# Performance work log

Hardware: AMD Instinct MI355X
Metric: run time of the kernel (lower is better)

## Reference

```python
import jax, jax.numpy as jnp
import numpy as np

B, V, D = 512, 50000, 512   # batch, vocab, embedding_dim
T, P, L, PL = 4, 16, 8, 32  # max_types, max_paths, max_pathlen, max_prop_len
OUT = 300


def masked_softmax(x):
    # zeros are treated as padding: add -9999 before softmax
    return jax.nn.softmax(x + jnp.where(x == 0, -9999.0, 0.0), axis=-1)


def cosine(a, b, eps=1e-8):
    na = jnp.maximum(jnp.linalg.norm(a, axis=1), eps)
    nb = jnp.maximum(jnp.linalg.norm(b, axis=1), eps)
    return jnp.sum(a * b, axis=1) / (na * nb)


def setup_inputs() -> dict:
    key = jax.random.key(0)
    ks = jax.random.split(key, 10)
    nodes = jax.random.randint(ks[0], (B, 2), 0, V)
    features = jax.random.randint(ks[1], (B, 2, T, P, L), 0, V)
    prop_nodes = jax.random.randint(ks[2], (B, 2), 0, V)
    prop_features = jax.random.randint(ks[3], (B, 2, 3, PL), 0, V)
    emb = jax.random.normal(ks[4], (V, D), dtype=jnp.float32)
    W_out = jax.random.normal(ks[5], (OUT, 2 * D), dtype=jnp.float32) * (1.0 / np.sqrt(2 * D))
    b_out = jnp.zeros((OUT,), dtype=jnp.float32)
    v = jnp.full((L,), 1.0 / L, dtype=jnp.float32)
    w_rootpath = jnp.array([0.25], dtype=jnp.float32)
    w_children = jnp.array([0.25], dtype=jnp.float32)
    w_obj_neighbours = jnp.array([0.25], dtype=jnp.float32)
    prop_weight = jnp.array([0.33], dtype=jnp.float32)
    domain_weight = jnp.array([0.33], dtype=jnp.float32)
    return dict(nodes=nodes, features=features, prop_nodes=prop_nodes,
                prop_features=prop_features, emb=emb, W_out=W_out, b_out=b_out,
                v=v, w_rootpath=w_rootpath, w_children=w_children,
                w_obj_neighbours=w_obj_neighbours, prop_weight=prop_weight,
                domain_weight=domain_weight)


def reference(nodes, features, prop_nodes, prop_features, emb, W_out, b_out,
              v, w_rootpath, w_children, w_obj_neighbours, prop_weight,
              domain_weight):
    results = []
    for i in range(2):  # the two siamese branches
        node_emb = emb[nodes[:, i]]                      # [B, D]
        feature_emb = emb[features[:, i]]                # [B, T, P, L, D]
        # score each path: dot every token with the node embedding, sum over pathlen
        path_weights = jnp.einsum('bd,btpld->btp', node_emb, feature_emb)  # [B,T,P]
        best = jnp.argmax(path_weights, axis=-1)         # [B, T]
        best_path = jnp.take_along_axis(
            feature_emb, best[:, :, None, None, None], axis=2).squeeze(2)  # [B,T,L,D]
        node_weights = masked_softmax(
            jnp.einsum('bd,btld->btl', node_emb, best_path))               # [B,T,L]
        attended = node_weights[..., None] * best_path                     # [B,T,L,D]
        dwp = jnp.einsum('l,btld->btd', v, attended)                       # [B,T,D]
        w_data = 1.0 - w_rootpath - w_children - w_obj_neighbours
        context = (w_rootpath * dwp[:, 0] + w_children * dwp[:, 1]
                   + w_obj_neighbours * dwp[:, 2] + w_data * dwp[:, 3])    # [B,D]
        contextual = jnp.concatenate([node_emb, context], axis=1)          # [B,2D]
        results.append(contextual @ W_out.T + b_out)                       # [B,300]
    sim_ent = cosine(results[0], results[1])                               # [B]
    # property branch (prop_nodes non-empty here)
    agg = emb[prop_features].sum(axis=-2)                                  # [B,2,3,D]
    sim_prop = (prop_weight * cosine(agg[:, 0, 0], agg[:, 1, 0])
                + domain_weight * cosine(agg[:, 0, 1], agg[:, 1, 1])
                + (1.0 - prop_weight - domain_weight) * cosine(agg[:, 0, 2], agg[:, 1, 2]))
    return jnp.concatenate([sim_ent, sim_prop])                            # [2B]
```

## Files before the change

kernel.cpp:

```cpp
#include <hip/hip_runtime.h>
#include <math.h>

#define B_ 512
#define V_ 50000
#define D_ 512
#define T_ 4
#define P_ 16
#define L_ 8
#define OUT_ 300
#define NBI 1024
#define NG  4096
#define NSLOT 524288
#define NSCAN 196

__global__ __launch_bounds__(256) void kprep(
    const int* __restrict__ features, int* __restrict__ counts,
    const int* __restrict__ nodes, const float* __restrict__ emb,
    float* __restrict__ narr, const float* __restrict__ W,
    float4* __restrict__ Wtv)
{
    const int blk = blockIdx.x;
    const int tid = threadIdx.x;
    if (blk < NSLOT / 256) {
        const int slot = blk * 256 + tid;
        atomicAdd(&counts[features[slot]], 1);
    } else if (blk < NSLOT / 256 + NBI) {
        const int bi = blk - NSLOT / 256;
        const float2 r = *(const float2*)(emb + (size_t)nodes[bi] * D_ + 2 * tid);
        *(float2*)(narr + (size_t)bi * D_ + 2 * tid) = r;
    } else {
        const int o = blk - NSLOT / 256 - NBI;
        const float4 w = *(const float4*)(W + (size_t)o * 1024 + 4 * tid);
        Wtv[(size_t)tid * OUT_ + o] = w;
    }
}

__global__ __launch_bounds__(256) void kb1_bsum(
    const int* __restrict__ counts, int* __restrict__ bsum)
{
    const int tid = threadIdx.x, v = blockIdx.x * 256 + tid;
    const int wid = tid >> 6, lane = tid & 63;
    __shared__ int red[4];
    int c = (v < V_) ? counts[v] : 0;
    #pragma unroll
    for (int off = 32; off; off >>= 1) c += __shfl_down(c, off);
    if (lane == 0) red[wid] = c;
    __syncthreads();
    if (tid == 0) bsum[blockIdx.x] = red[0] + red[1] + red[2] + red[3];
}

__global__ __launch_bounds__(256) void kb2_scan(
    const int* __restrict__ bsum, int* __restrict__ bbase)
{
    const int tid = threadIdx.x;
    __shared__ int sc[256];
    const int x = (tid < NSCAN) ? bsum[tid] : 0;
    sc[tid] = x;
    __syncthreads();
    for (int off = 1; off < 256; off <<= 1) {
        const int y = (tid >= off) ? sc[tid - off] : 0;
        __syncthreads();
        sc[tid] += y;
        __syncthreads();
    }
    if (tid < NSCAN) bbase[tid] = sc[tid] - x;
}

__global__ __launch_bounds__(256) void kb3_offsets(
    const int* __restrict__ counts, const int* __restrict__ bbase,
    int* __restrict__ offs, int* __restrict__ cursor)
{
    const int tid = threadIdx.x, v = blockIdx.x * 256 + tid;
    __shared__ int sc[256];
    const int c = (v < V_) ? counts[v] : 0;
    sc[tid] = c;
    __syncthreads();
    for (int off = 1; off < 256; off <<= 1) {
        const int y = (tid >= off) ? sc[tid - off] : 0;
        __syncthreads();
        sc[tid] += y;
        __syncthreads();
    }
    const int o = bbase[blockIdx.x] + sc[tid] - c;
    if (v < V_) { offs[v] = o; cursor[v] = o; }
    if (v == V_ - 1) offs[V_] = o + c;
}

__global__ __launch_bounds__(256) void kc_scatter(
    const int* __restrict__ features, int* __restrict__ cursor,
    int* __restrict__ inv)
{
    const int slot = blockIdx.x * 256 + threadIdx.x;
    const int row  = features[slot];
    const int pos  = atomicAdd(&cursor[row], 1);
    inv[pos] = slot;
}

__global__ __launch_bounds__(256) void kd_dots(
    const float* __restrict__ emb, const float* __restrict__ narr,
    const int* __restrict__ offs, const int* __restrict__ inv,
    float* __restrict__ sarr)
{
    const int tid = threadIdx.x;
    const int wid = tid >> 6, lane = tid & 63;
    const int row = blockIdx.x * 4 + wid;
    const int st = offs[row], en = offs[row + 1];
    if (st >= en) return;

    const float* rp = emb + (size_t)row * D_ + lane * 8;
    const float4 r0 = ((const float4*)rp)[0];
    const float4 r1 = ((const float4*)rp)[1];

    const int grp = lane >> 4;
    const int sub = lane & 15;
    const int eperm = (grp == 1) ? 2 : (grp == 2) ? 1 : grp;

    for (int e = st; e < en; e += 4) {
        int  s[4]; bool val[4];
        #pragma unroll
        for (int k = 0; k < 4; ++k) {
            val[k] = (e + k) < en;
            s[k]   = inv[val[k] ? (e + k) : (en - 1)];
        }
        float d[4];
        #pragma unroll
        for (int k = 0; k < 4; ++k) {
            const float* q = narr + (size_t)(s[k] >> 9) * D_ + lane * 8;
            const float4 a0 = ((const float4*)q)[0];
            const float4 a1 = ((const float4*)q)[1];
            d[k] = r0.x*a0.x + r0.y*a0.y + r0.z*a0.z + r0.w*a0.w
                 + r1.x*a1.x + r1.y*a1.y + r1.z*a1.z + r1.w*a1.w;
        }
        const bool b32 = (lane & 32) != 0;
        float c01 = (b32 ? d[1] : d[0]) + __shfl_xor(b32 ? d[0] : d[1], 32);
        float c23 = (b32 ? d[3] : d[2]) + __shfl_xor(b32 ? d[2] : d[3], 32);
        const bool b16 = (lane & 16) != 0;
        float c = (b16 ? c23 : c01) + __shfl_xor(b16 ? c01 : c23, 16);
        c += __shfl_xor(c, 8);
        c += __shfl_xor(c, 4);
        c += __shfl_xor(c, 2);
        c += __shfl_xor(c, 1);
        if (sub == 0 && val[eperm]) sarr[s[eperm]] = c;
    }
}

__global__ __launch_bounds__(256) void kef_sel_ctx(
    const float* __restrict__ sarr, const int* __restrict__ features,
    const int* __restrict__ nodes, const float* __restrict__ emb,
    const float* __restrict__ v, const float* __restrict__ w_rp,
    const float* __restrict__ w_ch, const float* __restrict__ w_on,
    float* __restrict__ cont)
{
    const int bi  = blockIdx.x;
    const int tid = threadIdx.x;
    const int wid = tid >> 6, lane = tid & 63;
    const int g = bi * 4 + wid;
    const int t = wid;

    __shared__ int   s_idx[32];
    __shared__ float s_coef[32];

    float bv = -1e30f; int bix = 0x7fffffff;
    if (lane < P_) {
        const float* sp = sarr + (size_t)g * 128 + lane * 8;
        const float4 x0 = ((const float4*)sp)[0];
        const float4 x1 = ((const float4*)sp)[1];
        bv = x0.x + x0.y + x0.z + x0.w + x1.x + x1.y + x1.z + x1.w;
        bix = lane;
    }
    #pragma unroll
    for (int off = 8; off; off >>= 1) {
        const float ov = __shfl_down(bv, off);
        const int   oi = __shfl_down(bix, off);
        if (ov > bv || (ov == bv && oi < bix)) { bv = ov; bix = oi; }
    }
    const int bp = __shfl(bix, 0);

    float sv = 0.f;
    if (lane < L_) sv = sarr[(size_t)g * 128 + bp * 8 + lane];
    float x = sv + (sv == 0.0f ? -9999.0f : 0.0f);
    float m = x;
    #pragma unroll
    for (int off = 4; off; off >>= 1) m = fmaxf(m, __shfl_xor(m, off));
    const float e = expf(x - m);
    float sum = e;
    #pragma unroll
    for (int off = 4; off; off >>= 1) sum += __shfl_xor(sum, off);

    if (lane < L_) {
        const float wr = w_rp[0], wc = w_ch[0], wo = w_on[0];
        const float tw = (t == 0) ? wr : (t == 1) ? wc : (t == 2) ? wo
                                       : (1.0f - wr - wc - wo);
        s_coef[wid * 8 + lane] = tw * v[lane] * (e / sum);
        s_idx [wid * 8 + lane] = features[(size_t)g * 128 + bp * 8 + lane];
    }
    __syncthreads();

    float2 c = {0.f, 0.f};
    #pragma unroll 8
    for (int r = 0; r < 32; ++r) {
        const int   idx = s_idx[r];
        const float cf  = s_coef[r];
        const float2 rr = *(const float2*)(emb + (size_t)idx * D_ + 2 * tid);
        c.x += cf * rr.x;
        c.y += cf * rr.y;
    }
    const float2 nn = *(const float2*)(emb + (size_t)nodes[bi] * D_ + 2 * tid);
    float* cp = cont + (size_t)bi * 1024;
    *(float2*)(cp + 2 * tid)       = nn;
    *(float2*)(cp + 512 + 2 * tid) = c;
}

__global__ __launch_bounds__(256) void kg_gemm_cos(
    const float* __restrict__ cont, const float4* __restrict__ Wtv,
    const float* __restrict__ bias, float* __restrict__ out)
{
    const int bb  = blockIdx.x;
    const int tid = threadIdx.x;
    const int wid = tid >> 6, lane = tid & 63;

    __shared__ float4 cs[1024];
    __shared__ float  red[4][6];

    const float* cb = cont + (size_t)bb * 4 * 1024;
    for (int idx = tid; idx < 4096; idx += 256) {
        const int vv = idx & 3, k = idx >> 2;
        ((float*)&cs[k])[vv] = cb[vv * 1024 + k];
    }
    __syncthreads();

    float p[6] = {0,0,0,0,0,0};
    #pragma unroll
    for (int pass = 0; pass < 2; ++pass) {
        const int o = tid + pass * 256;
        if (o < OUT_) {
            float4 acc = {0,0,0,0};
            const float4* wp = Wtv + o;
            #pragma unroll 4
            for (int k4 = 0; k4 < 256; ++k4) {
                const float4 wv = wp[(size_t)k4 * OUT_];
                const float4 c0 = cs[4*k4+0];
                const float4 c1 = cs[4*k4+1];
                const float4 c2 = cs[4*k4+2];
                const float4 c3 = cs[4*k4+3];
                acc.x += c0.x*wv.x + c1.x*wv.y + c2.x*wv.z + c3.x*wv.w;
                acc.y += c0.y*wv.x + c1.y*wv.y + c2.y*wv.z + c3.y*wv.w;
                acc.z += c0.z*wv.x + c1.z*wv.y + c2.z*wv.z + c3.z*wv.w;
                acc.w += c0.w*wv.x + c1.w*wv.y + c2.w*wv.z + c3.w*wv.w;
            }
            const float bo = bias[o];
            const float r0 = acc.x + bo, r1 = acc.y + bo;
            const float r2 = acc.z + bo, r3 = acc.w + bo;
            p[0] += r0 * r1; p[1] += r0 * r0; p[2] += r1 * r1;
            p[3] += r2 * r3; p[4] += r2 * r2; p[5] += r3 * r3;
        }
    }
    #pragma unroll
    for (int q = 0; q < 6; ++q) {
        #pragma unroll
        for (int off = 32; off; off >>= 1) p[q] += __shfl_down(p[q], off);
    }
    if (lane == 0) {
        #pragma unroll
        for (int q = 0; q < 6; ++q) red[wid][q] = p[q];
    }
    __syncthreads();
    if (tid < 2) {
        const int j = tid;
        float ab = 0.f, aa = 0.f, bbv = 0.f;
        #pragma unroll
        for (int w2 = 0; w2 < 4; ++w2) {
            ab  += red[w2][j*3+0];
            aa  += red[w2][j*3+1];
            bbv += red[w2][j*3+2];
        }
        const float na = fmaxf(sqrtf(aa),  1e-8f);
        const float nb = fmaxf(sqrtf(bbv), 1e-8f);
        out[bb * 2 + j] = ab / (na * nb);
    }
}

__global__ __launch_bounds__(256) void kh1_prop(
    const int* __restrict__ pf, const float* __restrict__ emb,
    float* __restrict__ pprt)
{
    const int bj  = blockIdx.x;
    const int b   = bj / 3, j = bj % 3;
    const int tid = threadIdx.x;
    const int d4   = tid & 127;
    const int half = tid >> 7;

    const int base0 = ((b * 2 + 0) * 3 + j) * 32;
    const int base1 = ((b * 2 + 1) * 3 + j) * 32;

    float4 accA = {0,0,0,0}, accB = {0,0,0,0};
    #pragma unroll 4
    for (int k = half; k < 32; k += 2) {
        const int ia = pf[base0 + k];
        const int ib = pf[base1 + k];
        const float4 ra = *(const float4*)(emb + (size_t)ia * D_ + 4 * d4);
        const float4 rb = *(const float4*)(emb + (size_t)ib * D_ + 4 * d4);
        accA.x += ra.x; accA.y += ra.y; accA.z += ra.z; accA.w += ra.w;
        accB.x += rb.x; accB.y += rb.y; accB.z += rb.z; accB.w += rb.w;
    }

    __shared__ float4 lA[128], lB[128];
    __shared__ float  red[2][3];
    if (half == 1) { lA[d4] = accA; lB[d4] = accB; }
    __syncthreads();

    float pab = 0.f, paa = 0.f, pbb = 0.f;
    if (half == 0) {
        const float4 oA = lA[d4], oB = lB[d4];
        const float ax = accA.x + oA.x, ay = accA.y + oA.y;
        const float az = accA.z + oA.z, aw = accA.w + oA.w;
        const float bx = accB.x + oB.x, by = accB.y + oB.y;
        const float bz = accB.z + oB.z, bw = accB.w + oB.w;
        pab = ax*bx + ay*by + az*bz + aw*bw;
        paa = ax*ax + ay*ay + az*az + aw*aw;
        pbb = bx*bx + by*by + bz*bz + bw*bw;
    }
    #pragma unroll
    for (int off = 32; off; off >>= 1) {
        pab += __shfl_down(pab, off);
        paa += __shfl_down(paa, off);
        pbb += __shfl_down(pbb, off);
    }
    if ((tid & 63) == 0 && tid < 128) {
        red[tid >> 6][0] = pab; red[tid >> 6][1] = paa; red[tid >> 6][2] = pbb;
    }
    __syncthreads();
    if (tid == 0) {
        pprt[bj * 3 + 0] = red[0][0] + red[1][0];
        pprt[bj * 3 + 1] = red[0][1] + red[1][1];
        pprt[bj * 3 + 2] = red[0][2] + red[1][2];
    }
}

__global__ __launch_bounds__(256) void kh2_prop(
    const float* __restrict__ pprt, const float* __restrict__ pw_,
    const float* __restrict__ dw_, float* __restrict__ out)
{
    const int b = blockIdx.x * 256 + threadIdx.x;
    if (b >= B_) return;
    float cosv[3];
    #pragma unroll
    for (int j = 0; j < 3; ++j) {
        const float ab = pprt[(b * 3 + j) * 3 + 0];
        const float aa = pprt[(b * 3 + j) * 3 + 1];
        const float bb = pprt[(b * 3 + j) * 3 + 2];
        const float na = fmaxf(sqrtf(aa), 1e-8f);
        const float nb = fmaxf(sqrtf(bb), 1e-8f);
        cosv[j] = ab / (na * nb);
    }
    const float pw = pw_[0], dw = dw_[0];
    out[B_ + b] = pw * cosv[0] + dw * cosv[1] + (1.0f - pw - dw) * cosv[2];
}

extern "C" void kernel_launch(void* const* d_in, const int* in_sizes, int n_in,
                              void* d_out, int out_size, void* d_ws, size_t ws_size,
                              hipStream_t stream) {
    const int*   nodes   = (const int*)  d_in[0];
    const int*   features= (const int*)  d_in[1];
    const int*   propf   = (const int*)  d_in[3];
    const float* emb     = (const float*)d_in[4];
    const float* W_out   = (const float*)d_in[5];
    const float* b_out   = (const float*)d_in[6];
    const float* v       = (const float*)d_in[7];
    const float* w_rp    = (const float*)d_in[8];
    const float* w_ch    = (const float*)d_in[9];
    const float* w_on    = (const float*)d_in[10];
    const float* pw      = (const float*)d_in[11];
    const float* dw      = (const float*)d_in[12];
    float* out = (float*)d_out;

    char* ws = (char*)d_ws;
    size_t o = 0;
    auto alloc = [&](size_t bytes) { char* p = ws + o; o += (bytes + 1023) & ~(size_t)1023; return p; };
    int*   counts = (int*)  alloc(V_ * 4);
    int*   offs   = (int*)  alloc((V_ + 1) * 4);
    int*   cursor = (int*)  alloc(V_ * 4);
    int*   bsum   = (int*)  alloc(NSCAN * 4);
    int*   bbase  = (int*)  alloc(NSCAN * 4);
    float* narr   = (float*)alloc((size_t)NBI * D_ * 4);
    int*   inv    = (int*)  alloc((size_t)NSLOT * 4);
    float* sarr   = (float*)alloc((size_t)NSLOT * 4);
    float* cont   = (float*)alloc((size_t)NBI * 1024 * 4);
    float* pprt   = (float*)alloc(B_ * 3 * 3 * 4);
    float4* Wtv   = (float4*)alloc((size_t)256 * OUT_ * 16);

    hipMemsetAsync(counts, 0, V_ * 4, stream);
    kprep      <<<NSLOT/256 + NBI + OUT_, 256, 0, stream>>>(
                  features, counts, nodes, emb, narr, W_out, Wtv);
    kb1_bsum   <<<NSCAN,      256, 0, stream>>>(counts, bsum);
    kb2_scan   <<<1,          256, 0, stream>>>(bsum, bbase);
    kb3_offsets<<<NSCAN,      256, 0, stream>>>(counts, bbase, offs, cursor);
    kc_scatter <<<NSLOT/256,  256, 0, stream>>>(features, cursor, inv);
    kd_dots    <<<V_/4,       256, 0, stream>>>(emb, narr, offs, inv, sarr);
    kef_sel_ctx<<<NBI,        256, 0, stream>>>(sarr, features, nodes, emb,
                                                v, w_rp, w_ch, w_on, cont);
    kg_gemm_cos<<<B_/2,       256, 0, stream>>>(cont, Wtv, b_out, out);
    kh1_prop   <<<B_*3,       256, 0, stream>>>(propf, emb, pprt);
    kh2_prop   <<<2,          256, 0, stream>>>(pprt, pw, dw, out);
}
```

Baseline: 235.2 us.

## Fuse property-branch kernels into dots and GEMM launches, unroll dot loop by eight

The property-sum kernel is merged into the per-row dot kernel as extra leading blocks, and the final property cosine kernel is merged into the GEMM/cosine kernel as two extra blocks. This removes two launches and lets the property gathers overlap with the dot-product work. The dot loop now handles eight entries per iteration, issuing all loads before computing, to raise memory-level parallelism. The cost is higher register pressure and shared memory that the dots path reserves but never uses.

```diff
diff --git a/kernel.cpp b/kernel.cpp
--- a/kernel.cpp
+++ b/kernel.cpp
@@ -12,6 +12,7 @@
 #define NG  4096
 #define NSLOT 524288
 #define NSCAN 196
+#define NPROPB 1536
 
 __global__ __launch_bounds__(256) void kprep(
     const int* __restrict__ features, int* __restrict__ counts,
@@ -96,14 +97,71 @@
     inv[pos] = slot;
 }
 
-__global__ __launch_bounds__(256) void kd_dots(
+__global__ __launch_bounds__(256) void kdh_dots_prop(
     const float* __restrict__ emb, const float* __restrict__ narr,
     const int* __restrict__ offs, const int* __restrict__ inv,
-    float* __restrict__ sarr)
-{
+    float* __restrict__ sarr,
+    const int* __restrict__ pf, float* __restrict__ pprt)
+{
+    const int blk = blockIdx.x;
     const int tid = threadIdx.x;
+
+    __shared__ float4 lA[128], lB[128];
+    __shared__ float  redp[2][3];
+
+    if (blk < NPROPB) {
+        const int bj  = blk;
+        const int b   = bj / 3, j = bj % 3;
+        const int d4   = tid & 127;
+        const int half = tid >> 7;
+
+        const int base0 = ((b * 2 + 0) * 3 + j) * 32;
+        const int base1 = ((b * 2 + 1) * 3 + j) * 32;
+
+        float4 accA = {0,0,0,0}, accB = {0,0,0,0};
+        #pragma unroll 4
+        for (int k = half; k < 32; k += 2) {
+            const int ia = pf[base0 + k];
+            const int ib = pf[base1 + k];
+            const float4 ra = *(const float4*)(emb + (size_t)ia * D_ + 4 * d4);
+            const float4 rb = *(const float4*)(emb + (size_t)ib * D_ + 4 * d4);
+            accA.x += ra.x; accA.y += ra.y; accA.z += ra.z; accA.w += ra.w;
+            accB.x += rb.x; accB.y += rb.y; accB.z += rb.z; accB.w += rb.w;
+        }
+        if (half == 1) { lA[d4] = accA; lB[d4] = accB; }
+        __syncthreads();
+
+        float pab = 0.f, paa = 0.f, pbb = 0.f;
+        if (half == 0) {
+            const float4 oA = lA[d4], oB = lB[d4];
+            const float ax = accA.x + oA.x, ay = accA.y + oA.y;
+            const float az = accA.z + oA.z, aw = accA.w + oA.w;
+            const float bx = accB.x + oB.x, by = accB.y + oB.y;
+            const float bz = accB.z + oB.z, bw = accB.w + oB.w;
+            pab = ax*bx + ay*by + az*bz + aw*bw;
+            paa = ax*ax + ay*ay + az*az + aw*aw;
+            pbb = bx*bx + by*by + bz*bz + bw*bw;
+        }
+        #pragma unroll
+        for (int off = 32; off; off >>= 1) {
+            pab += __shfl_down(pab, off);
+            paa += __shfl_down(paa, off);
+            pbb += __shfl_down(pbb, off);
+        }
+        if ((tid & 63) == 0 && tid < 128) {
+            redp[tid >> 6][0] = pab; redp[tid >> 6][1] = paa; redp[tid >> 6][2] = pbb;
+        }
+        __syncthreads();
+        if (tid == 0) {
+            pprt[bj * 3 + 0] = redp[0][0] + redp[1][0];
+            pprt[bj * 3 + 1] = redp[0][1] + redp[1][1];
+            pprt[bj * 3 + 2] = redp[0][2] + redp[1][2];
+        }
+        return;
+    }
+
     const int wid = tid >> 6, lane = tid & 63;
-    const int row = blockIdx.x * 4 + wid;
+    const int row = (blk - NPROPB) * 4 + wid;
     const int st = offs[row], en = offs[row + 1];
     if (st >= en) return;
 
@@ -115,32 +173,68 @@
     const int sub = lane & 15;
     const int eperm = (grp == 1) ? 2 : (grp == 2) ? 1 : grp;
 
-    for (int e = st; e < en; e += 4) {
-        int  s[4]; bool val[4];
+    for (int e = st; e < en; e += 8) {
+        const bool half2 = (e + 4) < en;
+        int  s0[4], s1[4]; bool v0[4], v1[4];
         #pragma unroll
         for (int k = 0; k < 4; ++k) {
-            val[k] = (e + k) < en;
-            s[k]   = inv[val[k] ? (e + k) : (en - 1)];
-        }
+            v0[k] = (e + k) < en;
+            s0[k] = inv[v0[k] ? (e + k) : (en - 1)];
+        }
+        #pragma unroll
+        for (int k = 0; k < 4; ++k) {
+            v1[k] = (e + 4 + k) < en;
+            s1[k] = inv[v1[k] ? (e + 4 + k) : (en - 1)];
+        }
+
+        float4 A0[4], A1[4], B0[4], B1[4];
+        #pragma unroll
+        for (int k = 0; k < 4; ++k) {
+            const float4* q = (const float4*)(narr + (size_t)(s0[k] >> 9) * D_ + lane * 8);
+            A0[k] = q[0]; A1[k] = q[1];
+        }
+        if (half2) {
+            #pragma unroll
+            for (int k = 0; k < 4; ++k) {
+                const float4* q = (const float4*)(narr + (size_t)(s1[k] >> 9) * D_ + lane * 8);
+                B0[k] = q[0]; B1[k] = q[1];
+            }
+        }
+
         float d[4];
         #pragma unroll
-        for (int k = 0; k < 4; ++k) {
-            const float* q = narr + (size_t)(s[k] >> 9) * D_ + lane * 8;
-            const float4 a0 = ((const float4*)q)[0];
-            const float4 a1 = ((const float4*)q)[1];
-            d[k] = r0.x*a0.x + r0.y*a0.y + r0.z*a0.z + r0.w*a0.w
-                 + r1.x*a1.x + r1.y*a1.y + r1.z*a1.z + r1.w*a1.w;
-        }
-        const bool b32 = (lane & 32) != 0;
-        float c01 = (b32 ? d[1] : d[0]) + __shfl_xor(b32 ? d[0] : d[1], 32);
-        float c23 = (b32 ? d[3] : d[2]) + __shfl_xor(b32 ? d[2] : d[3], 32);
-        const bool b16 = (lane & 16) != 0;
-        float c = (b16 ? c23 : c01) + __shfl_xor(b16 ? c01 : c23, 16);
-        c += __shfl_xor(c, 8);
-        c += __shfl_xor(c, 4);
-        c += __shfl_xor(c, 2);
-        c += __shfl_xor(c, 1);
-        if (sub == 0 && val[eperm]) sarr[s[eperm]] = c;
+        for (int k = 0; k < 4; ++k)
+            d[k] = r0.x*A0[k].x + r0.y*A0[k].y + r0.z*A0[k].z + r0.w*A0[k].w
+                 + r1.x*A1[k].x + r1.y*A1[k].y + r1.z*A1[k].z + r1.w*A1[k].w;
+        {
+            const bool b32 = (lane & 32) != 0;
+            float c01 = (b32 ? d[1] : d[0]) + __shfl_xor(b32 ? d[0] : d[1], 32);
+            float c23 = (b32 ? d[3] : d[2]) + __shfl_xor(b32 ? d[2] : d[3], 32);
+            const bool b16 = (lane & 16) != 0;
+            float c = (b16 ? c23 : c01) + __shfl_xor(b16 ? c01 : c23, 16);
+            c += __shfl_xor(c, 8);
+            c += __shfl_xor(c, 4);
+            c += __shfl_xor(c, 2);
+            c += __shfl_xor(c, 1);
+            if (sub == 0 && v0[eperm]) sarr[s0[eperm]] = c;
+        }
+        if (half2) {
+            float g[4];
+            #pragma unroll
+            for (int k = 0; k < 4; ++k)
+                g[k] = r0.x*B0[k].x + r0.y*B0[k].y + r0.z*B0[k].z + r0.w*B0[k].w
+                     + r1.x*B1[k].x + r1.y*B1[k].y + r1.z*B1[k].z + r1.w*B1[k].w;
+            const bool b32 = (lane & 32) != 0;
+            float c01 = (b32 ? g[1] : g[0]) + __shfl_xor(b32 ? g[0] : g[1], 32);
+            float c23 = (b32 ? g[3] : g[2]) + __shfl_xor(b32 ? g[2] : g[3], 32);
+            const bool b16 = (lane & 16) != 0;
+            float c = (b16 ? c23 : c01) + __shfl_xor(b16 ? c01 : c23, 16);
+            c += __shfl_xor(c, 8);
+            c += __shfl_xor(c, 4);
+            c += __shfl_xor(c, 2);
+            c += __shfl_xor(c, 1);
+            if (sub == 0 && v1[eperm]) sarr[s1[eperm]] = c;
+        }
     }
 }
 
@@ -213,10 +307,32 @@
 
 __global__ __launch_bounds__(256) void kg_gemm_cos(
     const float* __restrict__ cont, const float4* __restrict__ Wtv,
-    const float* __restrict__ bias, float* __restrict__ out)
+    const float* __restrict__ bias, const float* __restrict__ pprt,
+    const float* __restrict__ pw_, const float* __restrict__ dw_,
+    float* __restrict__ out)
 {
     const int bb  = blockIdx.x;
     const int tid = threadIdx.x;
+
+    if (bb >= B_ / 2) {
+        const int b = (bb - B_ / 2) * 256 + tid;
+        if (b < B_) {
+            float cosv[3];
+            #pragma unroll
+            for (int j = 0; j < 3; ++j) {
+                const float ab = pprt[(b * 3 + j) * 3 + 0];
+                const float aa = pprt[(b * 3 + j) * 3 + 1];
+                const float bv = pprt[(b * 3 + j) * 3 + 2];
+                const float na = fmaxf(sqrtf(aa), 1e-8f);
+                const float nb = fmaxf(sqrtf(bv), 1e-8f);
+                cosv[j] = ab / (na * nb);
+            }
+            const float pw = pw_[0], dw = dw_[0];
+            out[B_ + b] = pw * cosv[0] + dw * cosv[1] + (1.0f - pw - dw) * cosv[2];
+        }
+        return;
+    }
+
     const int wid = tid >> 6, lane = tid & 63;
 
     __shared__ float4 cs[1024];
@@ -280,83 +396,6 @@
     }
 }
 
-__global__ __launch_bounds__(256) void kh1_prop(
-    const int* __restrict__ pf, const float* __restrict__ emb,
-    float* __restrict__ pprt)
-{
-    const int bj  = blockIdx.x;
-    const int b   = bj / 3, j = bj % 3;
-    const int tid = threadIdx.x;
-    const int d4   = tid & 127;
-    const int half = tid >> 7;
-
-    const int base0 = ((b * 2 + 0) * 3 + j) * 32;
-    const int base1 = ((b * 2 + 1) * 3 + j) * 32;
-
-    float4 accA = {0,0,0,0}, accB = {0,0,0,0};
-    #pragma unroll 4
-    for (int k = half; k < 32; k += 2) {
-        const int ia = pf[base0 + k];
-        const int ib = pf[base1 + k];
-        const float4 ra = *(const float4*)(emb + (size_t)ia * D_ + 4 * d4);
-        const float4 rb = *(const float4*)(emb + (size_t)ib * D_ + 4 * d4);
-        accA.x += ra.x; accA.y += ra.y; accA.z += ra.z; accA.w += ra.w;
-        accB.x += rb.x; accB.y += rb.y; accB.z += rb.z; accB.w += rb.w;
-    }
-
-    __shared__ float4 lA[128], lB[128];
-    __shared__ float  red[2][3];
-    if (half == 1) { lA[d4] = accA; lB[d4] = accB; }
-    __syncthreads();
-
-    float pab = 0.f, paa = 0.f, pbb = 0.f;
-    if (half == 0) {
-        const float4 oA = lA[d4], oB = lB[d4];
-        const float ax = accA.x + oA.x, ay = accA.y + oA.y;
-        const float az = accA.z + oA.z, aw = accA.w + oA.w;
-        const float bx = accB.x + oB.x, by = accB.y + oB.y;
-        const float bz = accB.z + oB.z, bw = accB.w + oB.w;
-        pab = ax*bx + ay*by + az*bz + aw*bw;
-        paa = ax*ax + ay*ay + az*az + aw*aw;
-        pbb = bx*bx + by*by + bz*bz + bw*bw;
-    }
-    #pragma unroll
-    for (int off = 32; off; off >>= 1) {
-        pab += __shfl_down(pab, off);
-        paa += __shfl_down(paa, off);
-        pbb += __shfl_down(pbb, off);
-    }
-    if ((tid & 63) == 0 && tid < 128) {
-        red[tid >> 6][0] = pab; red[tid >> 6][1] = paa; red[tid >> 6][2] = pbb;
-    }
-    __syncthreads();
-    if (tid == 0) {
-        pprt[bj * 3 + 0] = red[0][0] + red[1][0];
-        pprt[bj * 3 + 1] = red[0][1] + red[1][1];
-        pprt[bj * 3 + 2] = red[0][2] + red[1][2];
-    }
-}
-
-__global__ __launch_bounds__(256) void kh2_prop(
-    const float* __restrict__ pprt, const float* __restrict__ pw_,
-    const float* __restrict__ dw_, float* __restrict__ out)
-{
-    const int b = blockIdx.x * 256 + threadIdx.x;
-    if (b >= B_) return;
-    float cosv[3];
-    #pragma unroll
-    for (int j = 0; j < 3; ++j) {
-        const float ab = pprt[(b * 3 + j) * 3 + 0];
-        const float aa = pprt[(b * 3 + j) * 3 + 1];
-        const float bb = pprt[(b * 3 + j) * 3 + 2];
-        const float na = fmaxf(sqrtf(aa), 1e-8f);
-        const float nb = fmaxf(sqrtf(bb), 1e-8f);
-        cosv[j] = ab / (na * nb);
-    }
-    const float pw = pw_[0], dw = dw_[0];
-    out[B_ + b] = pw * cosv[0] + dw * cosv[1] + (1.0f - pw - dw) * cosv[2];
-}
-
 extern "C" void kernel_launch(void* const* d_in, const int* in_sizes, int n_in,
                               void* d_out, int out_size, void* d_ws, size_t ws_size,
                               hipStream_t stream) {
@@ -390,16 +429,16 @@
     float4* Wtv   = (float4*)alloc((size_t)256 * OUT_ * 16);
 
     hipMemsetAsync(counts, 0, V_ * 4, stream);
-    kprep      <<<NSLOT/256 + NBI + OUT_, 256, 0, stream>>>(
-                  features, counts, nodes, emb, narr, W_out, Wtv);
-    kb1_bsum   <<<NSCAN,      256, 0, stream>>>(counts, bsum);
-    kb2_scan   <<<1,          256, 0, stream>>>(bsum, bbase);
-    kb3_offsets<<<NSCAN,      256, 0, stream>>>(counts, bbase, offs, cursor);
-    kc_scatter <<<NSLOT/256,  256, 0, stream>>>(features, cursor, inv);
-    kd_dots    <<<V_/4,       256, 0, stream>>>(emb, narr, offs, inv, sarr);
-    kef_sel_ctx<<<NBI,        256, 0, stream>>>(sarr, features, nodes, emb,
-                                                v, w_rp, w_ch, w_on, cont);
-    kg_gemm_cos<<<B_/2,       256, 0, stream>>>(cont, Wtv, b_out, out);
-    kh1_prop   <<<B_*3,       256, 0, stream>>>(propf, emb, pprt);
-    kh2_prop   <<<2,          256, 0, stream>>>(pprt, pw, dw, out);
-}
+    kprep       <<<NSLOT/256 + NBI + OUT_, 256, 0, stream>>>(
+                   features, counts, nodes, emb, narr, W_out, Wtv);
+    kb1_bsum    <<<NSCAN,           256, 0, stream>>>(counts, bsum);
+    kb2_scan    <<<1,               256, 0, stream>>>(bsum, bbase);
+    kb3_offsets <<<NSCAN,           256, 0, stream>>>(counts, bbase, offs, cursor);
+    kc_scatter  <<<NSLOT/256,       256, 0, stream>>>(features, cursor, inv);
+    kdh_dots_prop<<<NPROPB + V_/4,  256, 0, stream>>>(emb, narr, offs, inv, sarr,
+                                                      propf, pprt);
+    kef_sel_ctx <<<NBI,             256, 0, stream>>>(sarr, features, nodes, emb,
+                                                      v, w_rp, w_ch, w_on, cont);
+    kg_gemm_cos <<<B_/2 + 2,        256, 0, stream>>>(cont, Wtv, b_out, pprt,
+                                                      pw, dw, out);
+}
```

Measured after the change: 233.5 us. About the same (-0.7%).
